# Kernel tuning notes

Measured on AMD Instinct MI355X. Metric: run time of the kernel, lower is better.

Reference implementation:

```python
import jax, jax.numpy as jnp
import numpy as np

C, G, S, L, B = 16, 8192, 8, 3, 32


def setup_inputs() -> dict:
    key = jax.random.key(0)
    kx, kI = jax.random.split(key)
    # x: valuation vector over G ground atoms per batch element, in [0,1)
    x = jax.random.uniform(kx, (B, G), dtype=jnp.float32)
    # I: precomputed index tensor [C, G, S, L], indices into the G axis of x
    I = jax.random.randint(kI, (C, G, S, L), 0, G, dtype=jnp.int64)
    return {"x": x, "I": I}


def reference(x, I):
    # Equivalent of: for each clause i, gather(V_tild, 1, I_i) -> prod over L -> sum over S
    # torch gather semantics: out[b, g, s, l] = x[b, I[i, g, s, l]]
    # Vectorized over all clauses at once; no repeat/broadcast materialization beyond the gather.
    gathered = x[:, I]                        # [B, C, G, S, L]
    body = jnp.prod(gathered, axis=-1)        # conjunction over L body literals -> [B, C, G, S]
    clause_val = jnp.sum(body, axis=-1)       # sum over S substitutions -> [B, C, G]
    # torch.stack over clauses puts C first: [C, B, G]
    return jnp.transpose(clause_val, (1, 0, 2))
```

## Files before the change

### kernel.cpp

```cpp
#include <hip/hip_runtime.h>
#include <hip/hip_fp16.h>
#include <stdint.h>

#define Cc 16
#define Gg 8192
#define Ss 8
#define Ll 3
#define Bb 32

#define ZS 4
#define THREADS 1024
#define ITERS 2

__device__ __forceinline__ void clause_eval(const uint2* __restrict__ xl2,
                                            const int4 q[6], float acc[8]) {
    #pragma unroll
    for (int h = 0; h < 2; ++h) {
        const int4 qa = q[3 * h + 0];
        const int4 qb = q[3 * h + 1];
        const int4 qc = q[3 * h + 2];
        int idx[12] = {qa.x, qa.y, qa.z, qa.w,
                       qb.x, qb.y, qb.z, qb.w,
                       qc.x, qc.y, qc.z, qc.w};
        uint2 r0[12], r1[12];
        #pragma unroll
        for (int k = 0; k < 12; ++k) {
            uint32_t u = (uint32_t)idx[k];
            uint32_t a0 = (u << 1) | ((u >> 3) & 1u);
            r0[k] = xl2[a0];
            r1[k] = xl2[a0 ^ 1u];
        }
        #pragma unroll
        for (int s = 0; s < 4; ++s) {
            const int k0 = 3 * s, k1 = 3 * s + 1, k2 = 3 * s + 2;
            const uint32_t pa[4] = {r0[k0].x, r0[k0].y, r1[k0].x, r1[k0].y};
            const uint32_t pb[4] = {r0[k1].x, r0[k1].y, r1[k1].x, r1[k1].y};
            const uint32_t pd[4] = {r0[k2].x, r0[k2].y, r1[k2].x, r1[k2].y};
            #pragma unroll
            for (int j = 0; j < 4; ++j) {
                __half2 a = *(const __half2*)&pa[j];
                __half2 b = *(const __half2*)&pb[j];
                __half2 d = *(const __half2*)&pd[j];
                __half2 p = __hmul2(__hmul2(a, b), d);
                float2 pf = __half22float2(p);
                acc[2 * j]     += pf.x;
                acc[2 * j + 1] += pf.y;
            }
        }
    }
}

__global__ __launch_bounds__(THREADS, 4) void clause_f16_fused(
        const float* __restrict__ x, const int* __restrict__ I,
        float* __restrict__ out) {
    __shared__ uint4 xl[Gg];
    const int tid = threadIdx.x;

    const int lb = (blockIdx.x & 7) * 32 + (blockIdx.x >> 3);
    const int c = lb >> 4;
    const int z = (lb >> 2) & 3;
    const int gbase = (lb & 3) * (THREADS * ITERS);

    const int g0 = gbase + tid;
    const int g1 = gbase + THREADS + tid;
    const int4* ip0 = (const int4*)(I + ((size_t)c * Gg + g0) * (Ss * Ll));
    const int4* ip1 = (const int4*)(I + ((size_t)c * Gg + g1) * (Ss * Ll));
    int4 q0[6], q1[6];
    #pragma unroll
    for (int k = 0; k < 6; ++k) q0[k] = ip0[k];
    #pragma unroll
    for (int k = 0; k < 6; ++k) q1[k] = ip1[k];

    {
        const float* xs = x + (size_t)(8 * z) * Gg;
        #pragma unroll 4
        for (int k = 0; k < 8; ++k) {
            const int g = tid + k * THREADS;
            float v[8];
            #pragma unroll
            for (int b = 0; b < 8; ++b) v[b] = xs[(size_t)b * Gg + g];
            uint32_t d[4];
            #pragma unroll
            for (int j = 0; j < 4; ++j) {
                __half2 h = __floats2half2_rn(v[2 * j], v[2 * j + 1]);
                d[j] = *(const uint32_t*)&h;
            }
            const uint32_t s = (g >> 3) & 1u;
            xl[g] = s ? make_uint4(d[2], d[3], d[0], d[1])
                      : make_uint4(d[0], d[1], d[2], d[3]);
        }
    }

    __syncthreads();

    const uint2* xl2 = (const uint2*)xl;
    float* opb = out + ((size_t)(c * Bb + 8 * z)) * Gg;

    {
        float acc[8] = {0, 0, 0, 0, 0, 0, 0, 0};
        clause_eval(xl2, q0, acc);
        #pragma unroll
        for (int j = 0; j < 8; ++j)
            opb[(size_t)j * Gg + g0] = acc[j];
    }
    {
        float acc[8] = {0, 0, 0, 0, 0, 0, 0, 0};
        clause_eval(xl2, q1, acc);
        #pragma unroll
        for (int j = 0; j < 8; ++j)
            opb[(size_t)j * Gg + g1] = acc[j];
    }
}

extern "C" void kernel_launch(void* const* d_in, const int* in_sizes, int n_in,
                              void* d_out, int out_size, void* d_ws, size_t ws_size,
                              hipStream_t stream) {
    const float* x = (const float*)d_in[0];
    const int* I = (const int*)d_in[1];
    float* out = (float*)d_out;
    (void)d_ws; (void)ws_size;

    const int grid = (Cc * Gg * ZS) / (THREADS * ITERS);
    clause_f16_fused<<<grid, THREADS, 0, stream>>>(x, I, out);
}
```

Before: 80.74 us.

## Split batch into 4-wide slices with 64KB LDS table and 512-thread blocks

```diff
diff --git a/kernel.cpp b/kernel.cpp
--- a/kernel.cpp
+++ b/kernel.cpp
@@ -8,12 +8,15 @@
 #define Ll 3
 #define Bb 32
 
-#define ZS 4
-#define THREADS 1024
+#define BH 4
+#define NZ (Bb / BH)
+#define THREADS 512
 #define ITERS 2
+#define GCH (THREADS * ITERS)
+#define NGC (Gg / GCH)
 
 __device__ __forceinline__ void clause_eval(const uint2* __restrict__ xl2,
-                                            const int4 q[6], float acc[8]) {
+                                            const int4 q[6], float acc[4]) {
     #pragma unroll
     for (int h = 0; h < 2; ++h) {
         const int4 qa = q[3 * h + 0];
@@ -22,44 +25,42 @@
         int idx[12] = {qa.x, qa.y, qa.z, qa.w,
                        qb.x, qb.y, qb.z, qb.w,
                        qc.x, qc.y, qc.z, qc.w};
-        uint2 r0[12], r1[12];
+        uint2 r[12];
         #pragma unroll
-        for (int k = 0; k < 12; ++k) {
-            uint32_t u = (uint32_t)idx[k];
-            uint32_t a0 = (u << 1) | ((u >> 3) & 1u);
-            r0[k] = xl2[a0];
-            r1[k] = xl2[a0 ^ 1u];
-        }
+        for (int k = 0; k < 12; ++k)
+            r[k] = xl2[(uint32_t)idx[k]];
         #pragma unroll
         for (int s = 0; s < 4; ++s) {
-            const int k0 = 3 * s, k1 = 3 * s + 1, k2 = 3 * s + 2;
-            const uint32_t pa[4] = {r0[k0].x, r0[k0].y, r1[k0].x, r1[k0].y};
-            const uint32_t pb[4] = {r0[k1].x, r0[k1].y, r1[k1].x, r1[k1].y};
-            const uint32_t pd[4] = {r0[k2].x, r0[k2].y, r1[k2].x, r1[k2].y};
-            #pragma unroll
-            for (int j = 0; j < 4; ++j) {
-                __half2 a = *(const __half2*)&pa[j];
-                __half2 b = *(const __half2*)&pb[j];
-                __half2 d = *(const __half2*)&pd[j];
-                __half2 p = __hmul2(__hmul2(a, b), d);
-                float2 pf = __half22float2(p);
-                acc[2 * j]     += pf.x;
-                acc[2 * j + 1] += pf.y;
-            }
+            const uint2 ra = r[3 * s + 0];
+            const uint2 rb = r[3 * s + 1];
+            const uint2 rd = r[3 * s + 2];
+            __half2 p0 = __hmul2(__hmul2(*(const __half2*)&ra.x,
+                                         *(const __half2*)&rb.x),
+                                 *(const __half2*)&rd.x);
+            __half2 p1 = __hmul2(__hmul2(*(const __half2*)&ra.y,
+                                         *(const __half2*)&rb.y),
+                                 *(const __half2*)&rd.y);
+            float2 f0 = __half22float2(p0);
+            float2 f1 = __half22float2(p1);
+            acc[0] += f0.x;
+            acc[1] += f0.y;
+            acc[2] += f1.x;
+            acc[3] += f1.y;
         }
     }
 }
 
-__global__ __launch_bounds__(THREADS, 4) void clause_f16_fused(
+__global__ __launch_bounds__(THREADS, 4) void clause_f16_p2(
         const float* __restrict__ x, const int* __restrict__ I,
         float* __restrict__ out) {
-    __shared__ uint4 xl[Gg];
+    __shared__ uint2 xl[Gg];
     const int tid = threadIdx.x;
 
-    const int lb = (blockIdx.x & 7) * 32 + (blockIdx.x >> 3);
-    const int c = lb >> 4;
-    const int z = (lb >> 2) & 3;
-    const int gbase = (lb & 3) * (THREADS * ITERS);
+    const int lb = (blockIdx.x & 7) * (1024 / 8) + (blockIdx.x >> 3);
+    const int zh = lb & (NZ - 1);
+    const int gc = (lb >> 3) & (NGC - 1);
+    const int c  = lb >> 6;
+    const int gbase = gc * GCH;
 
     const int g0 = gbase + tid;
     const int g1 = gbase + THREADS + tid;
@@ -72,42 +73,40 @@
     for (int k = 0; k < 6; ++k) q1[k] = ip1[k];
 
     {
-        const float* xs = x + (size_t)(8 * z) * Gg;
+        const float* xs = x + (size_t)(BH * zh) * Gg;
         #pragma unroll 4
-        for (int k = 0; k < 8; ++k) {
-            const int g = tid + k * THREADS;
-            float v[8];
-            #pragma unroll
-            for (int b = 0; b < 8; ++b) v[b] = xs[(size_t)b * Gg + g];
-            uint32_t d[4];
-            #pragma unroll
-            for (int j = 0; j < 4; ++j) {
-                __half2 h = __floats2half2_rn(v[2 * j], v[2 * j + 1]);
-                d[j] = *(const uint32_t*)&h;
-            }
-            const uint32_t s = (g >> 3) & 1u;
-            xl[g] = s ? make_uint4(d[2], d[3], d[0], d[1])
-                      : make_uint4(d[0], d[1], d[2], d[3]);
+        for (int k = 0; k < Gg / (2 * THREADS); ++k) {
+            const int g = 2 * (tid + k * THREADS);
+            float2 v0 = *(const float2*)&xs[g];
+            float2 v1 = *(const float2*)&xs[Gg + g];
+            float2 v2 = *(const float2*)&xs[2 * (size_t)Gg + g];
+            float2 v3 = *(const float2*)&xs[3 * (size_t)Gg + g];
+            __half2 a01 = __floats2half2_rn(v0.x, v1.x);
+            __half2 a23 = __floats2half2_rn(v2.x, v3.x);
+            __half2 b01 = __floats2half2_rn(v0.y, v1.y);
+            __half2 b23 = __floats2half2_rn(v2.y, v3.y);
+            uint4 w = make_uint4(*(const uint32_t*)&a01, *(const uint32_t*)&a23,
+                                 *(const uint32_t*)&b01, *(const uint32_t*)&b23);
+            *(uint4*)&xl[g] = w;
         }
     }
 
     __syncthreads();
 
-    const uint2* xl2 = (const uint2*)xl;
-    float* opb = out + ((size_t)(c * Bb + 8 * z)) * Gg;
+    float* opb = out + ((size_t)(c * Bb + BH * zh)) * Gg;
 
     {
-        float acc[8] = {0, 0, 0, 0, 0, 0, 0, 0};
-        clause_eval(xl2, q0, acc);
+        float acc[4] = {0, 0, 0, 0};
+        clause_eval(xl, q0, acc);
         #pragma unroll
-        for (int j = 0; j < 8; ++j)
+        for (int j = 0; j < 4; ++j)
             opb[(size_t)j * Gg + g0] = acc[j];
     }
     {
-        float acc[8] = {0, 0, 0, 0, 0, 0, 0, 0};
-        clause_eval(xl2, q1, acc);
+        float acc[4] = {0, 0, 0, 0};
+        clause_eval(xl, q1, acc);
         #pragma unroll
-        for (int j = 0; j < 8; ++j)
+        for (int j = 0; j < 4; ++j)
             opb[(size_t)j * Gg + g1] = acc[j];
     }
 }
@@ -120,6 +119,6 @@
     float* out = (float*)d_out;
     (void)d_ws; (void)ws_size;
 
-    const int grid = (Cc * Gg * ZS) / (THREADS * ITERS);
-    clause_f16_fused<<<grid, THREADS, 0, stream>>>(x, I, out);
+    const int grid = Cc * NGC * NZ;
+    clause_f16_p2<<<grid, THREADS, 0, stream>>>(x, I, out);
 }
```

Result: no change. 81.01 us (+0.3%).
